# Kernel optimization log

Measured on AMD Instinct MI355X. Metric: run time of the kernel, lower is better.

Reference implementation:

```python
import jax, jax.numpy as jnp
import numpy as np

B, N, F_IN, H, C = 32768, 12, 128, 4, 64  # batch, nodes/graph, input_dim, heads, hidden_dim
NEG_SLOPE = 0.2  # PyG GATConv default leaky_relu slope


def setup_inputs() -> dict:
    key = jax.random.key(0)
    ks = jax.random.split(key, 16)
    def xavier(k, shape):
        fan_in, fan_out = shape[0], int(np.prod(shape[1:]))
        lim = float(np.sqrt(6.0 / (fan_in + fan_out)))
        return jax.random.uniform(k, shape, jnp.float32, -lim, lim)
    return {
        "node_features": jax.random.normal(ks[0], (B, N, F_IN), jnp.float32),
        "W1": xavier(ks[1], (F_IN, H, C)),
        "a_src1": xavier(ks[2], (H, C)),
        "a_dst1": xavier(ks[3], (H, C)),
        "b1": jnp.zeros((H * C,), jnp.float32),
        "W2": xavier(ks[4], (H * C, 1, C)),
        "a_src2": xavier(ks[5], (1, C)),
        "a_dst2": xavier(ks[6], (1, C)),
        "b2": jnp.zeros((C,), jnp.float32),
        # classifier head: 64 -> 32 -> 1
        "Wc1": xavier(ks[7], (C, C // 2)),
        "bc1": jnp.zeros((C // 2,), jnp.float32),
        "Wc2": xavier(ks[8], (C // 2, 1)),
        "bc2": jnp.zeros((1,), jnp.float32),
    }


def gat_dense(x, W, a_src, a_dst, bias, concat):
    # x: [B, N, F].  Fully-connected graph + self-loops (PyG GATConv default)
    # == dense attention over all N nodes of each graph.
    h = jnp.einsum("bnf,fhc->bnhc", x, W)               # [B,N,H,C]
    e_src = jnp.einsum("bnhc,hc->bnh", h, a_src)         # alpha contrib of source j
    e_dst = jnp.einsum("bnhc,hc->bnh", h, a_dst)         # alpha contrib of target i
    # edge (j -> i): logit = leaky_relu(e_dst[i] + e_src[j])
    logits = jax.nn.leaky_relu(e_dst[:, :, None, :] + e_src[:, None, :, :], NEG_SLOPE)  # [B,i,j,H]
    alpha = jax.nn.softmax(logits, axis=2)               # softmax over neighbors j
    out = jnp.einsum("bijh,bjhc->bihc", alpha, h)        # aggregate
    if concat:
        out = out.reshape(out.shape[0], out.shape[1], -1)
    else:
        out = out.mean(axis=2)
    return out + bias


def reference(node_features, W1, a_src1, a_dst1, b1, W2, a_src2, a_dst2, b2,
              Wc1, bc1, Wc2, bc2):
    # eval mode: dropouts are identity; is_finetune=False so finetune_block skipped
    x = jax.nn.elu(gat_dense(node_features, W1, a_src1, a_dst1, b1, concat=True))   # [B,N,256]
    x = jax.nn.elu(gat_dense(x, W2, a_src2, a_dst2, b2, concat=False))              # [B,N,64]
    g = x.mean(axis=1)                                                              # global_mean_pool -> [B,64]
    hdn = jax.nn.relu(g @ Wc1 + bc1)
    logits = hdn @ Wc2 + bc2                                                        # [B,1]
    return logits
```

## Files before the change

### kernel.cpp

```cpp
#include <hip/hip_runtime.h>
#include <math.h>

typedef __attribute__((ext_vector_type(8))) short bf16x8;
typedef __attribute__((ext_vector_type(4))) float f32x4;

namespace {
constexpr int NN  = 12;
constexpr int FIN = 128;
constexpr int D1  = 256;
constexpr int C2  = 64;
constexpr float SLOPE = 0.2f;

__device__ __forceinline__ unsigned short f2bf(float f) {
    unsigned u = __builtin_bit_cast(unsigned, f);
    u += 0x7FFFu + ((u >> 16) & 1u);
    return (unsigned short)(u >> 16);
}
__device__ __forceinline__ float elu1(float x) { return x > 0.f ? x : __expf(x) - 1.f; }
__device__ __forceinline__ float lrelu(float x) { return x > 0.f ? x : SLOPE * x; }
}

__global__ void prep_weights(const float* __restrict__ W1, const float* __restrict__ as1,
                             const float* __restrict__ ad1,
                             const float* __restrict__ W2, const float* __restrict__ as2,
                             const float* __restrict__ ad2,
                             unsigned short* __restrict__ wsB1, unsigned short* __restrict__ wsB2) {
    int t = blockIdx.x * 256 + threadIdx.x;
    if (t < 34816) {
        int i = t & 7, l = (t >> 3) & 63, kn = t >> 9;
        int kt = kn / 17, nt = kn % 17;
        int k = kt * 32 + (l >> 4) * 8 + i;
        float v = 0.f;
        if (nt < 16) {
            v = W1[k * 256 + nt * 16 + (l & 15)];
        } else {
            int cc = l & 15;
            if (cc < 4)      for (int c = 0; c < 64; ++c) v += W1[k * 256 + cc * 64 + c] * as1[cc * 64 + c];
            else if (cc < 8) for (int c = 0; c < 64; ++c) v += W1[k * 256 + (cc - 4) * 64 + c] * ad1[(cc - 4) * 64 + c];
        }
        wsB1[t] = f2bf(v);
    } else if (t < 55296) {
        int t2 = t - 34816;
        int i = t2 & 7, l = (t2 >> 3) & 63, kn = t2 >> 9;
        int kt = kn / 5, nt = kn % 5;
        int k = kt * 32 + (l >> 4) * 8 + i;
        float v = 0.f;
        if (nt < 4) {
            v = W2[k * 64 + nt * 16 + (l & 15)];
        } else {
            int cc = l & 15;
            if (cc == 0)      for (int c = 0; c < 64; ++c) v += W2[k * 64 + c] * as2[c];
            else if (cc == 1) for (int c = 0; c < 64; ++c) v += W2[k * 64 + c] * ad2[c];
        }
        wsB2[t2] = f2bf(v);
    }
}

__global__ __launch_bounds__(256, 2) void gat_mfma5(
    const float* __restrict__ x_in,
    const unsigned short* __restrict__ wsB1,
    const unsigned short* __restrict__ wsB2,
    const float* __restrict__ b1, const float* __restrict__ b2,
    const float* __restrict__ Wc1, const float* __restrict__ bc1,
    const float* __restrict__ Wc2, const float* __restrict__ bc2,
    float* __restrict__ out)
{
    __shared__ __align__(16) unsigned char R0[13056];
    __shared__ __align__(16) unsigned char R1[32768];
    __shared__ __align__(16) unsigned char R2[24576];
    __shared__ float eS1[48][4], eD1[48][4];
    __shared__ float eS2[48], eD2[48];
    __shared__ float gpool[4][64];

    const int b = blockIdx.x, t = threadIdx.x;
    const int w = t >> 6, l = t & 63, l15 = l & 15, lq = l >> 4;

    {
        const float4* xs = (const float4*)(x_in + (size_t)b * (4 * NN * FIN));
        #pragma unroll
        for (int it = 0; it < 6; ++it) {
            int q = t + 256 * it;
            float4 v = xs[q];
            int e0 = q << 2, r = e0 >> 7, k = e0 & 127;
            int addr = ((r << 8) + (k << 1)) ^ ((r & 7) << 4);
            unsigned p0 = (unsigned)f2bf(v.x) | ((unsigned)f2bf(v.y) << 16);
            unsigned p1 = (unsigned)f2bf(v.z) | ((unsigned)f2bf(v.w) << 16);
            *(uint2*)(R0 + addr) = make_uint2(p0, p1);
        }
        #pragma unroll
        for (int it = 0; it < 6; ++it)
            *(uint4*)(R2 + ((it * 256 + t) << 4)) = make_uint4(0, 0, 0, 0);
        #pragma unroll
        for (int z = 0; z < 2; ++z) {
            int id = t + 256 * z;
            int col = id >> 1, bs = 6 + (id & 1);
            int addr = ((col << 7) + (bs << 4)) ^ ((col & 7) << 4);
            *(uint4*)(R1 + addr) = make_uint4(0, 0, 0, 0);
        }
    }
    __syncthreads();

    {
        const uint4* pb = (const uint4*)wsB1;
        bf16x8 Bf[4][4];
        #pragma unroll
        for (int ng = 0; ng < 4; ++ng)
            #pragma unroll
            for (int kt = 0; kt < 4; ++kt)
                Bf[ng][kt] = __builtin_bit_cast(bf16x8, pb[(kt * 17 + (w * 4 + ng)) * 64 + l]);
        bf16x8 Bfe[4];
        if (w == 0) {
            #pragma unroll
            for (int kt = 0; kt < 4; ++kt)
                Bfe[kt] = __builtin_bit_cast(bf16x8, pb[(kt * 17 + 16) * 64 + l]);
        }
        #pragma unroll
        for (int m = 0; m < 3; ++m) {
            int r = m * 16 + l15, abase = (r << 8) + (lq << 4), swz = (r & 7) << 4;
            bf16x8 Af[4];
            #pragma unroll
            for (int kt = 0; kt < 4; ++kt)
                Af[kt] = *(const bf16x8*)(R0 + ((abase + (kt << 6)) ^ swz));
            f32x4 acc[4];
            #pragma unroll
            for (int ng = 0; ng < 4; ++ng) acc[ng] = (f32x4){0.f, 0.f, 0.f, 0.f};
            #pragma unroll
            for (int ng = 0; ng < 4; ++ng)
                #pragma unroll
                for (int kt = 0; kt < 4; ++kt)
                    acc[ng] = __builtin_amdgcn_mfma_f32_16x16x32_bf16(Af[kt], Bf[ng][kt], acc[ng], 0, 0, 0);
            int row0 = m * 16 + lq * 4;
            #pragma unroll
            for (int ng = 0; ng < 4; ++ng) {
                int col = w * 64 + ng * 16 + l15;
                unsigned q0 = (unsigned)f2bf(acc[ng][0]) | ((unsigned)f2bf(acc[ng][1]) << 16);
                unsigned q1 = (unsigned)f2bf(acc[ng][2]) | ((unsigned)f2bf(acc[ng][3]) << 16);
                int addr = ((col << 7) + (row0 << 1)) ^ ((col & 7) << 4);
                *(uint2*)(R1 + addr) = make_uint2(q0, q1);
            }
            if (w == 0) {
                f32x4 acce = (f32x4){0.f, 0.f, 0.f, 0.f};
                #pragma unroll
                for (int kt = 0; kt < 4; ++kt)
                    acce = __builtin_amdgcn_mfma_f32_16x16x32_bf16(Af[kt], Bfe[kt], acce, 0, 0, 0);
                if (l15 < 8) {
                    #pragma unroll
                    for (int reg = 0; reg < 4; ++reg) {
                        int row = row0 + reg;
                        if (l15 < 4) eS1[row][l15] = acce[reg];
                        else         eD1[row][l15 - 4] = acce[reg];
                    }
                }
            }
        }
    }
    __syncthreads();

    if (t < 192) {
        int g = t / 48, rem = t % 48, i = rem >> 2, h = rem & 3;
        int rowi = g * 12 + i;
        float edi = eD1[rowi][h];
        float lv[12]; float mx = -1e30f;
        #pragma unroll
        for (int j = 0; j < 12; ++j) {
            float v = lrelu(edi + eS1[g * 12 + j][h]);
            lv[j] = v; mx = fmaxf(mx, v);
        }
        float s = 0.f;
        #pragma unroll
        for (int j = 0; j < 12; ++j) { lv[j] = __expf(lv[j] - mx); s += lv[j]; }
        float inv = 1.f / s;
        unsigned char* base = R2 + h * 6144;
        int rb = rowi << 7, swz = (rowi & 7) << 4, ob = g * 24;
        #pragma unroll
        for (int p = 0; p < 3; ++p) {
            unsigned q0 = (unsigned)f2bf(lv[4*p]   * inv) | ((unsigned)f2bf(lv[4*p+1] * inv) << 16);
            unsigned q1 = (unsigned)f2bf(lv[4*p+2] * inv) | ((unsigned)f2bf(lv[4*p+3] * inv) << 16);
            int addr = (rb + ob + p * 8) ^ swz;
            *(uint2*)(base + addr) = make_uint2(q0, q1);
        }
    }
    __syncthreads();

    {
        bf16x8 Bh[2][4];
        #pragma unroll
        for (int kt = 0; kt < 2; ++kt)
            #pragma unroll
            for (int nt = 0; nt < 4; ++nt) {
                int col = w * 64 + nt * 16 + l15;
                int addr = ((col << 7) + (kt << 6) + (lq << 4)) ^ ((col & 7) << 4);
                Bh[kt][nt] = *(const bf16x8*)(R1 + addr);
            }
        float b1v[4];
        #pragma unroll
        for (int nt = 0; nt < 4; ++nt) b1v[nt] = b1[w * 64 + nt * 16 + l15];
        unsigned char* aab = R2 + w * 6144;
        #pragma unroll
        for (int m = 0; m < 3; ++m) {
            int r = m * 16 + l15, swz = (r & 7) << 4;
            bf16x8 Aa[2];
            #pragma unroll
            for (int kt = 0; kt < 2; ++kt)
                Aa[kt] = *(const bf16x8*)(aab + (((r << 7) + (kt << 6) + (lq << 4)) ^ swz));
            #pragma unroll
            for (int nt = 0; nt < 4; ++nt) {
                f32x4 acc = (f32x4){0.f, 0.f, 0.f, 0.f};
                #pragma unroll
                for (int kt = 0; kt < 2; ++kt)
                    acc = __builtin_amdgcn_mfma_f32_16x16x32_bf16(Aa[kt], Bh[kt][nt], acc, 0, 0, 0);
                #pragma unroll
                for (int reg = 0; reg < 4; ++reg) {
                    int row = m * 16 + lq * 4 + reg;
                    float val = elu1(acc[reg] + b1v[nt]);
                    int addr = ((row << 7) + ((nt * 16 + l15) << 1)) ^ ((row & 7) << 4);
                    *(unsigned short*)(aab + addr) = f2bf(val);
                }
            }
        }
    }
    __syncthreads();

    {
        if (t < 128) {
            int col = t >> 1, bs = 6 + (t & 1);
            int addr = ((col << 7) + (bs << 4)) ^ ((col & 7) << 4);
            *(uint4*)(R1 + addr) = make_uint4(0, 0, 0, 0);
        }
        if (t < 192) {
            *(uint4*)(R1 + 8192 + (t << 4)) = make_uint4(0, 0, 0, 0);
            *(uint4*)(R1 + 8192 + ((t + 192) << 4)) = make_uint4(0, 0, 0, 0);
        }
        const uint4* pb2 = (const uint4*)wsB2;
        bf16x8 Bg[8], Be2[8];
        #pragma unroll
        for (int kt = 0; kt < 8; ++kt)
            Bg[kt] = __builtin_bit_cast(bf16x8, pb2[(kt * 5 + w) * 64 + l]);
        if (w == 0) {
            #pragma unroll
            for (int kt = 0; kt < 8; ++kt)
                Be2[kt] = __builtin_bit_cast(bf16x8, pb2[(kt * 5 + 4) * 64 + l]);
        }
        #pragma unroll
        for (int m = 0; m < 3; ++m) {
            int r = m * 16 + l15, swz = (r & 7) << 4;
            f32x4 acc = (f32x4){0.f, 0.f, 0.f, 0.f}, acce = (f32x4){0.f, 0.f, 0.f, 0.f};
            #pragma unroll
            for (int kt = 0; kt < 8; ++kt) {
                int addr = (kt >> 1) * 6144 + (((r << 7) + ((kt & 1) << 6) + (lq << 4)) ^ swz);
                bf16x8 Ax = *(const bf16x8*)(R2 + addr);
                acc = __builtin_amdgcn_mfma_f32_16x16x32_bf16(Ax, Bg[kt], acc, 0, 0, 0);
                if (w == 0) acce = __builtin_amdgcn_mfma_f32_16x16x32_bf16(Ax, Be2[kt], acce, 0, 0, 0);
            }
            int col = w * 16 + l15, row0 = m * 16 + lq * 4;
            unsigned q0 = (unsigned)f2bf(acc[0]) | ((unsigned)f2bf(acc[1]) << 16);
            unsigned q1 = (unsigned)f2bf(acc[2]) | ((unsigned)f2bf(acc[3]) << 16);
            int addr = ((col << 7) + (row0 << 1)) ^ ((col & 7) << 4);
            *(uint2*)(R1 + addr) = make_uint2(q0, q1);
            if (w == 0 && l15 < 2) {
                #pragma unroll
                for (int reg = 0; reg < 4; ++reg) {
                    int row = row0 + reg;
                    if (l15 == 0) eS2[row] = acce[reg];
                    else          eD2[row] = acce[reg];
                }
            }
        }
    }
    __syncthreads();

    if (t < 48) {
        int g = t / 12;
        float edi = eD2[t];
        float lv[12]; float mx = -1e30f;
        #pragma unroll
        for (int j = 0; j < 12; ++j) {
            float v = lrelu(edi + eS2[g * 12 + j]);
            lv[j] = v; mx = fmaxf(mx, v);
        }
        float s = 0.f;
        #pragma unroll
        for (int j = 0; j < 12; ++j) { lv[j] = __expf(lv[j] - mx); s += lv[j]; }
        float inv = 1.f / s;
        int rb = t << 7, swz = (t & 7) << 4, ob = g * 24;
        #pragma unroll
        for (int p = 0; p < 3; ++p) {
            unsigned q0 = (unsigned)f2bf(lv[4*p]   * inv) | ((unsigned)f2bf(lv[4*p+1] * inv) << 16);
            unsigned q1 = (unsigned)f2bf(lv[4*p+2] * inv) | ((unsigned)f2bf(lv[4*p+3] * inv) << 16);
            int addr = 8192 + ((rb + ob + p * 8) ^ swz);
            *(uint2*)(R1 + addr) = make_uint2(q0, q1);
        }
    }
    __syncthreads();

    {
        bf16x8 Bh2[2];
        int col = w * 16 + l15;
        #pragma unroll
        for (int kt = 0; kt < 2; ++kt) {
            int addr = ((col << 7) + (kt << 6) + (lq << 4)) ^ ((col & 7) << 4);
            Bh2[kt] = *(const bf16x8*)(R1 + addr);
        }
        float b2v = b2[col];
        #pragma unroll
        for (int m = 0; m < 3; ++m) {
            int r = m * 16 + l15, swz = (r & 7) << 4;
            f32x4 acc = (f32x4){0.f, 0.f, 0.f, 0.f};
            #pragma unroll
            for (int kt = 0; kt < 2; ++kt) {
                bf16x8 Aa = *(const bf16x8*)(R1 + 8192 + (((r << 7) + (kt << 6) + (lq << 4)) ^ swz));
                acc = __builtin_amdgcn_mfma_f32_16x16x32_bf16(Aa, Bh2[kt], acc, 0, 0, 0);
            }
            #pragma unroll
            for (int reg = 0; reg < 4; ++reg) {
                int row = m * 16 + lq * 4 + reg;
                *(float*)(R0 + row * 272 + (col << 2)) = elu1(acc[reg] + b2v);
            }
        }
    }
    __syncthreads();

    {
        int o = t & 63, g = t >> 6;
        float s = 0.f;
        #pragma unroll
        for (int j = 0; j < 12; ++j)
            s += *(const float*)(R0 + (g * 12 + j) * 272 + (o << 2));
        gpool[g][o] = s * (1.0f / 12.0f);
    }
    __syncthreads();

    if (t < 128) {
        int g = t >> 5, nr = t & 31;
        float acc = bc1[nr];
        #pragma unroll
        for (int cc = 0; cc < 64; ++cc)
            acc = fmaf(gpool[g][cc], Wc1[cc * 32 + nr], acc);
        float val = fmaxf(acc, 0.f) * Wc2[nr];
        #pragma unroll
        for (int msk = 1; msk < 32; msk <<= 1) val += __shfl_xor(val, msk);
        if (nr == 0) out[b * 4 + g] = val + bc2[0];
    }
}

__global__ __launch_bounds__(256, 4) void gat_fused_f32(
    const float* __restrict__ x_in, const float* __restrict__ W1,
    const float* __restrict__ a_src1, const float* __restrict__ a_dst1,
    const float* __restrict__ b1, const float* __restrict__ W2,
    const float* __restrict__ a_src2, const float* __restrict__ a_dst2,
    const float* __restrict__ b2, const float* __restrict__ Wc1,
    const float* __restrict__ bc1, const float* __restrict__ Wc2,
    const float* __restrict__ bc2, float* __restrict__ out)
{
    __shared__ union {
        float x_l[NN][FIN];
        struct { float h2[NN][C2]; float x3[NN][C2]; } s2;
    } u;
    __shared__ float h1s[NN][D1];
    __shared__ float x2s[NN][D1];
    __shared__ float alpha1[NN][NN][4];
    __shared__ float e_s1[NN][4], e_d1[NN][4];
    __shared__ float e_s2[NN], e_d2[NN];
    __shared__ float alpha2[NN][NN];
    __shared__ float gph[C2];
    __shared__ float hdn[32];

    const int b = blockIdx.x, t = threadIdx.x;
    const float* xb = x_in + (size_t)b * (NN * FIN);
    for (int i = t; i < NN * FIN; i += 256) (&u.x_l[0][0])[i] = xb[i];
    __syncthreads();
    {
        const int o0 = (t & 127) * 2, n0 = (t >> 7) * 6;
        float acc[6][2];
        #pragma unroll
        for (int i = 0; i < 6; ++i) { acc[i][0] = 0.f; acc[i][1] = 0.f; }
        for (int f = 0; f < FIN; f += 4) {
            float4 xv[6];
            #pragma unroll
            for (int i = 0; i < 6; ++i) xv[i] = *(const float4*)&u.x_l[n0 + i][f];
            #pragma unroll
            for (int k = 0; k < 4; ++k) {
                const float2 wv = *(const float2*)&W1[(f + k) * D1 + o0];
                #pragma unroll
                for (int i = 0; i < 6; ++i) {
                    const float xs = ((const float*)&xv[i])[k];
                    acc[i][0] = fmaf(xs, wv.x, acc[i][0]);
                    acc[i][1] = fmaf(xs, wv.y, acc[i][1]);
                }
            }
        }
        #pragma unroll
        for (int i = 0; i < 6; ++i) { h1s[n0+i][o0] = acc[i][0]; h1s[n0+i][o0+1] = acc[i][1]; }
    }
    __syncthreads();
    if (t < NN * 4) {
        const int n = t >> 2, h = t & 3;
        float es = 0.f, ed = 0.f;
        for (int c = 0; c < 64; ++c) {
            const float v = h1s[n][h * 64 + c];
            es = fmaf(v, a_src1[h * 64 + c], es);
            ed = fmaf(v, a_dst1[h * 64 + c], ed);
        }
        e_s1[n][h] = es; e_d1[n][h] = ed;
    }
    __syncthreads();
    if (t < NN * 4) {
        const int i = t >> 2, h = t & 3;
        const float edi = e_d1[i][h];
        float lv[NN]; float m = -1e30f;
        #pragma unroll
        for (int j = 0; j < NN; ++j) {
            float v = edi + e_s1[j][h]; v = v > 0.f ? v : SLOPE * v;
            lv[j] = v; m = fmaxf(m, v);
        }
        float s = 0.f;
        #pragma unroll
        for (int j = 0; j < NN; ++j) { lv[j] = __expf(lv[j] - m); s += lv[j]; }
        const float inv = 1.f / s;
        #pragma unroll
        for (int j = 0; j < NN; ++j) alpha1[i][j][h] = lv[j] * inv;
    }
    __syncthreads();
    {
        const int o = t, h = o >> 6;
        const float bo = b1[o];
        float v[NN];
        #pragma unroll
        for (int j = 0; j < NN; ++j) v[j] = h1s[j][o];
        #pragma unroll
        for (int i = 0; i < NN; ++i) {
            float acc = 0.f;
            #pragma unroll
            for (int j = 0; j < NN; ++j) acc = fmaf(alpha1[i][j][h], v[j], acc);
            x2s[i][o] = acc + bo > 0.f ? acc + bo : expm1f(acc + bo);
        }
    }
    __syncthreads();
    {
        const int c = t & 63, n0 = (t >> 6) * 3;
        float acc[3] = {0.f, 0.f, 0.f};
        for (int f = 0; f < D1; f += 4) {
            float4 xv[3];
            #pragma unroll
            for (int i = 0; i < 3; ++i) xv[i] = *(const float4*)&x2s[n0 + i][f];
            #pragma unroll
            for (int k = 0; k < 4; ++k) {
                const float wv = W2[(f + k) * C2 + c];
                #pragma unroll
                for (int i = 0; i < 3; ++i) acc[i] = fmaf(((const float*)&xv[i])[k], wv, acc[i]);
            }
        }
        #pragma unroll
        for (int i = 0; i < 3; ++i) u.s2.h2[n0 + i][c] = acc[i];
    }
    __syncthreads();
    if (t < NN) {
        float es = 0.f, ed = 0.f;
        for (int c = 0; c < 64; c += 4) {
            const float4 v  = *(const float4*)&u.s2.h2[t][c];
            const float4 as = *(const float4*)&a_src2[c];
            const float4 ad = *(const float4*)&a_dst2[c];
            es += v.x*as.x + v.y*as.y + v.z*as.z + v.w*as.w;
            ed += v.x*ad.x + v.y*ad.y + v.z*ad.z + v.w*ad.w;
        }
        e_s2[t] = es; e_d2[t] = ed;
    }
    __syncthreads();
    if (t < NN) {
        const float edi = e_d2[t];
        float lv[NN]; float m = -1e30f;
        #pragma unroll
        for (int j = 0; j < NN; ++j) {
            float v = edi + e_s2[j]; v = v > 0.f ? v : SLOPE * v;
            lv[j] = v; m = fmaxf(m, v);
        }
        float s = 0.f;
        #pragma unroll
        for (int j = 0; j < NN; ++j) { lv[j] = __expf(lv[j] - m); s += lv[j]; }
        const float inv = 1.f / s;
        #pragma unroll
        for (int j = 0; j < NN; ++j) alpha2[t][j] = lv[j] * inv;
    }
    __syncthreads();
    {
        const int c = t & 63, i0 = (t >> 6) * 3;
        float v[NN];
        #pragma unroll
        for (int j = 0; j < NN; ++j) v[j] = u.s2.h2[j][c];
        const float bc = b2[c];
        #pragma unroll
        for (int ii = 0; ii < 3; ++ii) {
            const int i = i0 + ii;
            float acc = 0.f;
            #pragma unroll
            for (int j = 0; j < NN; ++j) acc = fmaf(alpha2[i][j], v[j], acc);
            u.s2.x3[i][c] = acc + bc > 0.f ? acc + bc : expm1f(acc + bc);
        }
    }
    __syncthreads();
    if (t < C2) {
        float s = 0.f;
        #pragma unroll
        for (int i = 0; i < NN; ++i) s += u.s2.x3[i][t];
        gph[t] = s * (1.0f / NN);
    }
    __syncthreads();
    if (t < 32) {
        float acc = bc1[t];
        for (int c = 0; c < C2; ++c) acc = fmaf(gph[c], Wc1[c * 32 + t], acc);
        hdn[t] = fmaxf(acc, 0.f);
    }
    __syncthreads();
    if (t == 0) {
        float acc = bc2[0];
        #pragma unroll
        for (int k = 0; k < 32; ++k) acc = fmaf(hdn[k], Wc2[k], acc);
        out[b] = acc;
    }
}

extern "C" void kernel_launch(void* const* d_in, const int* in_sizes, int n_in,
                              void* d_out, int out_size, void* d_ws, size_t ws_size,
                              hipStream_t stream) {
    const float* x   = (const float*)d_in[0];
    const float* W1  = (const float*)d_in[1];
    const float* as1 = (const float*)d_in[2];
    const float* ad1 = (const float*)d_in[3];
    const float* b1  = (const float*)d_in[4];
    const float* W2  = (const float*)d_in[5];
    const float* as2 = (const float*)d_in[6];
    const float* ad2 = (const float*)d_in[7];
    const float* b2  = (const float*)d_in[8];
    const float* Wc1 = (const float*)d_in[9];
    const float* bc1 = (const float*)d_in[10];
    const float* Wc2 = (const float*)d_in[11];
    const float* bc2 = (const float*)d_in[12];
    float* out = (float*)d_out;

    const int B = in_sizes[0] / (NN * FIN);

    if (ws_size >= 110592 && (B % 4) == 0) {
        unsigned short* wsB1 = (unsigned short*)d_ws;
        unsigned short* wsB2 = wsB1 + 34816;
        prep_weights<<<216, 256, 0, stream>>>(W1, as1, ad1, W2, as2, ad2, wsB1, wsB2);
        gat_mfma5<<<B / 4, 256, 0, stream>>>(x, wsB1, wsB2, b1, b2, Wc1, bc1, Wc2, bc2, out);
    } else {
        gat_fused_f32<<<B, 256, 0, stream>>>(x, W1, as1, ad1, b1, W2, as2, ad2, b2,
                                             Wc1, bc1, Wc2, bc2, out);
    }
}
```

Before: 169.2 us.

## Split per-block GAT work across eight waves instead of four

Moves the fused GAT kernel from 256 to 512 threads per block and redistributes every MFMA stage across the eight waves. Layer-1 column groups are split in half per wave, the aggregation step buffers A fragments and adds a barrier before writing back in place, and layer-2's fifteen (tile,row) units are spread two per wave. The goal is more waves per block for better latency hiding and shorter per-wave serial MFMA chains. In exchange it adds a barrier, leaves some waves idle in later stages, and may hurt occupancy through register and LDS limits under the new launch bounds.

```diff
diff --git a/kernel.cpp b/kernel.cpp
--- a/kernel.cpp
+++ b/kernel.cpp
@@ -56,7 +56,7 @@
     }
 }
 
-__global__ __launch_bounds__(256, 2) void gat_mfma5(
+__global__ __launch_bounds__(512, 4) void gat_mfma6(
     const float* __restrict__ x_in,
     const unsigned short* __restrict__ wsB1,
     const unsigned short* __restrict__ wsB2,
@@ -78,8 +78,8 @@
     {
         const float4* xs = (const float4*)(x_in + (size_t)b * (4 * NN * FIN));
         #pragma unroll
-        for (int it = 0; it < 6; ++it) {
-            int q = t + 256 * it;
+        for (int it = 0; it < 3; ++it) {
+            int q = t + 512 * it;
             float4 v = xs[q];
             int e0 = q << 2, r = e0 >> 7, k = e0 & 127;
             int addr = ((r << 8) + (k << 1)) ^ ((r & 7) << 4);
@@ -88,12 +88,10 @@
             *(uint2*)(R0 + addr) = make_uint2(p0, p1);
         }
         #pragma unroll
-        for (int it = 0; it < 6; ++it)
-            *(uint4*)(R2 + ((it * 256 + t) << 4)) = make_uint4(0, 0, 0, 0);
-        #pragma unroll
-        for (int z = 0; z < 2; ++z) {
-            int id = t + 256 * z;
-            int col = id >> 1, bs = 6 + (id & 1);
+        for (int it = 0; it < 3; ++it)
+            *(uint4*)(R2 + ((it * 512 + t) << 4)) = make_uint4(0, 0, 0, 0);
+        {
+            int col = t >> 1, bs = 6 + (t & 1);
             int addr = ((col << 7) + (bs << 4)) ^ ((col & 7) << 4);
             *(uint4*)(R1 + addr) = make_uint4(0, 0, 0, 0);
         }
@@ -102,12 +100,13 @@
 
     {
         const uint4* pb = (const uint4*)wsB1;
-        bf16x8 Bf[4][4];
-        #pragma unroll
-        for (int ng = 0; ng < 4; ++ng)
+        const int h = w >> 1, half = w & 1;
+        bf16x8 Bf[2][4];
+        #pragma unroll
+        for (int ngl = 0; ngl < 2; ++ngl)
             #pragma unroll
             for (int kt = 0; kt < 4; ++kt)
-                Bf[ng][kt] = __builtin_bit_cast(bf16x8, pb[(kt * 17 + (w * 4 + ng)) * 64 + l]);
+                Bf[ngl][kt] = __builtin_bit_cast(bf16x8, pb[(kt * 17 + (h * 4 + half * 2 + ngl)) * 64 + l]);
         bf16x8 Bfe[4];
         if (w == 0) {
             #pragma unroll
@@ -121,20 +120,20 @@
             #pragma unroll
             for (int kt = 0; kt < 4; ++kt)
                 Af[kt] = *(const bf16x8*)(R0 + ((abase + (kt << 6)) ^ swz));
-            f32x4 acc[4];
-            #pragma unroll
-            for (int ng = 0; ng < 4; ++ng) acc[ng] = (f32x4){0.f, 0.f, 0.f, 0.f};
-            #pragma unroll
-            for (int ng = 0; ng < 4; ++ng)
+            f32x4 acc[2];
+            #pragma unroll
+            for (int ngl = 0; ngl < 2; ++ngl) acc[ngl] = (f32x4){0.f, 0.f, 0.f, 0.f};
+            #pragma unroll
+            for (int ngl = 0; ngl < 2; ++ngl)
                 #pragma unroll
                 for (int kt = 0; kt < 4; ++kt)
-                    acc[ng] = __builtin_amdgcn_mfma_f32_16x16x32_bf16(Af[kt], Bf[ng][kt], acc[ng], 0, 0, 0);
+                    acc[ngl] = __builtin_amdgcn_mfma_f32_16x16x32_bf16(Af[kt], Bf[ngl][kt], acc[ngl], 0, 0, 0);
             int row0 = m * 16 + lq * 4;
             #pragma unroll
-            for (int ng = 0; ng < 4; ++ng) {
-                int col = w * 64 + ng * 16 + l15;
-                unsigned q0 = (unsigned)f2bf(acc[ng][0]) | ((unsigned)f2bf(acc[ng][1]) << 16);
-                unsigned q1 = (unsigned)f2bf(acc[ng][2]) | ((unsigned)f2bf(acc[ng][3]) << 16);
+            for (int ngl = 0; ngl < 2; ++ngl) {
+                int col = h * 64 + (half * 2 + ngl) * 16 + l15;
+                unsigned q0 = (unsigned)f2bf(acc[ngl][0]) | ((unsigned)f2bf(acc[ngl][1]) << 16);
+                unsigned q1 = (unsigned)f2bf(acc[ngl][2]) | ((unsigned)f2bf(acc[ngl][3]) << 16);
                 int addr = ((col << 7) + (row0 << 1)) ^ ((col & 7) << 4);
                 *(uint2*)(R1 + addr) = make_uint2(q0, q1);
             }
@@ -183,37 +182,42 @@
     __syncthreads();
 
     {
-        bf16x8 Bh[2][4];
+        const int h = w >> 1, half = w & 1;
+        bf16x8 Bh[2][2];
         #pragma unroll
         for (int kt = 0; kt < 2; ++kt)
             #pragma unroll
-            for (int nt = 0; nt < 4; ++nt) {
-                int col = w * 64 + nt * 16 + l15;
+            for (int ntl = 0; ntl < 2; ++ntl) {
+                int col = h * 64 + (half * 2 + ntl) * 16 + l15;
                 int addr = ((col << 7) + (kt << 6) + (lq << 4)) ^ ((col & 7) << 4);
-                Bh[kt][nt] = *(const bf16x8*)(R1 + addr);
-            }
-        float b1v[4];
-        #pragma unroll
-        for (int nt = 0; nt < 4; ++nt) b1v[nt] = b1[w * 64 + nt * 16 + l15];
-        unsigned char* aab = R2 + w * 6144;
+                Bh[kt][ntl] = *(const bf16x8*)(R1 + addr);
+            }
+        float b1v[2];
+        #pragma unroll
+        for (int ntl = 0; ntl < 2; ++ntl) b1v[ntl] = b1[h * 64 + (half * 2 + ntl) * 16 + l15];
+        unsigned char* aab = R2 + h * 6144;
+        bf16x8 Aa[3][2];
         #pragma unroll
         for (int m = 0; m < 3; ++m) {
             int r = m * 16 + l15, swz = (r & 7) << 4;
-            bf16x8 Aa[2];
             #pragma unroll
             for (int kt = 0; kt < 2; ++kt)
-                Aa[kt] = *(const bf16x8*)(aab + (((r << 7) + (kt << 6) + (lq << 4)) ^ swz));
-            #pragma unroll
-            for (int nt = 0; nt < 4; ++nt) {
+                Aa[m][kt] = *(const bf16x8*)(aab + (((r << 7) + (kt << 6) + (lq << 4)) ^ swz));
+        }
+        __syncthreads();
+        #pragma unroll
+        for (int m = 0; m < 3; ++m) {
+            #pragma unroll
+            for (int ntl = 0; ntl < 2; ++ntl) {
                 f32x4 acc = (f32x4){0.f, 0.f, 0.f, 0.f};
                 #pragma unroll
                 for (int kt = 0; kt < 2; ++kt)
-                    acc = __builtin_amdgcn_mfma_f32_16x16x32_bf16(Aa[kt], Bh[kt][nt], acc, 0, 0, 0);
+                    acc = __builtin_amdgcn_mfma_f32_16x16x32_bf16(Aa[m][kt], Bh[kt][ntl], acc, 0, 0, 0);
                 #pragma unroll
                 for (int reg = 0; reg < 4; ++reg) {
                     int row = m * 16 + lq * 4 + reg;
-                    float val = elu1(acc[reg] + b1v[nt]);
-                    int addr = ((row << 7) + ((nt * 16 + l15) << 1)) ^ ((row & 7) << 4);
+                    float val = elu1(acc[reg] + b1v[ntl]);
+                    int addr = ((row << 7) + (((half * 2 + ntl) * 16 + l15) << 1)) ^ ((row & 7) << 4);
                     *(unsigned short*)(aab + addr) = f2bf(val);
                 }
             }
@@ -232,37 +236,37 @@
             *(uint4*)(R1 + 8192 + ((t + 192) << 4)) = make_uint4(0, 0, 0, 0);
         }
         const uint4* pb2 = (const uint4*)wsB2;
-        bf16x8 Bg[8], Be2[8];
-        #pragma unroll
-        for (int kt = 0; kt < 8; ++kt)
-            Bg[kt] = __builtin_bit_cast(bf16x8, pb2[(kt * 5 + w) * 64 + l]);
-        if (w == 0) {
-            #pragma unroll
-            for (int kt = 0; kt < 8; ++kt)
-                Be2[kt] = __builtin_bit_cast(bf16x8, pb2[(kt * 5 + 4) * 64 + l]);
-        }
-        #pragma unroll
-        for (int m = 0; m < 3; ++m) {
-            int r = m * 16 + l15, swz = (r & 7) << 4;
-            f32x4 acc = (f32x4){0.f, 0.f, 0.f, 0.f}, acce = (f32x4){0.f, 0.f, 0.f, 0.f};
-            #pragma unroll
-            for (int kt = 0; kt < 8; ++kt) {
-                int addr = (kt >> 1) * 6144 + (((r << 7) + ((kt & 1) << 6) + (lq << 4)) ^ swz);
-                bf16x8 Ax = *(const bf16x8*)(R2 + addr);
-                acc = __builtin_amdgcn_mfma_f32_16x16x32_bf16(Ax, Bg[kt], acc, 0, 0, 0);
-                if (w == 0) acce = __builtin_amdgcn_mfma_f32_16x16x32_bf16(Ax, Be2[kt], acce, 0, 0, 0);
-            }
-            int col = w * 16 + l15, row0 = m * 16 + lq * 4;
-            unsigned q0 = (unsigned)f2bf(acc[0]) | ((unsigned)f2bf(acc[1]) << 16);
-            unsigned q1 = (unsigned)f2bf(acc[2]) | ((unsigned)f2bf(acc[3]) << 16);
-            int addr = ((col << 7) + (row0 << 1)) ^ ((col & 7) << 4);
-            *(uint2*)(R1 + addr) = make_uint2(q0, q1);
-            if (w == 0 && l15 < 2) {
-                #pragma unroll
-                for (int reg = 0; reg < 4; ++reg) {
-                    int row = row0 + reg;
-                    if (l15 == 0) eS2[row] = acce[reg];
-                    else          eD2[row] = acce[reg];
+        #pragma unroll
+        for (int ui = 0; ui < 2; ++ui) {
+            int u = w * 2 + ui;
+            if (u < 15) {
+                int tile = u / 3, m = u % 3;
+                bf16x8 Bg[8];
+                #pragma unroll
+                for (int kt = 0; kt < 8; ++kt)
+                    Bg[kt] = __builtin_bit_cast(bf16x8, pb2[(kt * 5 + tile) * 64 + l]);
+                int r = m * 16 + l15, swz = (r & 7) << 4;
+                f32x4 acc = (f32x4){0.f, 0.f, 0.f, 0.f};
+                #pragma unroll
+                for (int kt = 0; kt < 8; ++kt) {
+                    int addr = (kt >> 1) * 6144 + (((r << 7) + ((kt & 1) << 6) + (lq << 4)) ^ swz);
+                    bf16x8 Ax = *(const bf16x8*)(R2 + addr);
+                    acc = __builtin_amdgcn_mfma_f32_16x16x32_bf16(Ax, Bg[kt], acc, 0, 0, 0);
+                }
+                int row0 = m * 16 + lq * 4;
+                if (tile < 4) {
+                    int col = tile * 16 + l15;
+                    unsigned q0 = (unsigned)f2bf(acc[0]) | ((unsigned)f2bf(acc[1]) << 16);
+                    unsigned q1 = (unsigned)f2bf(acc[2]) | ((unsigned)f2bf(acc[3]) << 16);
+                    int addr = ((col << 7) + (row0 << 1)) ^ ((col & 7) << 4);
+                    *(uint2*)(R1 + addr) = make_uint2(q0, q1);
+                } else if (l15 < 2) {
+                    #pragma unroll
+                    for (int reg = 0; reg < 4; ++reg) {
+                        int row = row0 + reg;
+                        if (l15 == 0) eS2[row] = acc[reg];
+                        else          eD2[row] = acc[reg];
+                    }
                 }
             }
         }
@@ -294,16 +298,18 @@
     __syncthreads();
 
     {
+        const int otile = w & 3;
         bf16x8 Bh2[2];
-        int col = w * 16 + l15;
+        int col = otile * 16 + l15;
         #pragma unroll
         for (int kt = 0; kt < 2; ++kt) {
             int addr = ((col << 7) + (kt << 6) + (lq << 4)) ^ ((col & 7) << 4);
             Bh2[kt] = *(const bf16x8*)(R1 + addr);
         }
         float b2v = b2[col];
-        #pragma unroll
-        for (int m = 0; m < 3; ++m) {
+        const int m0 = (w < 4) ? 0 : 2, mcount = (w < 4) ? 2 : 1;
+        for (int mi = 0; mi < mcount; ++mi) {
+            int m = m0 + mi;
             int r = m * 16 + l15, swz = (r & 7) << 4;
             f32x4 acc = (f32x4){0.f, 0.f, 0.f, 0.f};
             #pragma unroll
@@ -320,7 +326,7 @@
     }
     __syncthreads();
 
-    {
+    if (t < 256) {
         int o = t & 63, g = t >> 6;
         float s = 0.f;
         #pragma unroll
@@ -543,7 +549,7 @@
         unsigned short* wsB1 = (unsigned short*)d_ws;
         unsigned short* wsB2 = wsB1 + 34816;
         prep_weights<<<216, 256, 0, stream>>>(W1, as1, ad1, W2, as2, ad2, wsB1, wsB2);
-        gat_mfma5<<<B / 4, 256, 0, stream>>>(x, wsB1, wsB2, b1, b2, Wc1, bc1, Wc2, bc2, out);
+        gat_mfma6<<<B / 4, 512, 0, stream>>>(x, wsB1, wsB2, b1, b2, Wc1, bc1, Wc2, bc2, out);
     } else {
         gat_fused_f32<<<B, 256, 0, stream>>>(x, W1, as1, ad1, b1, W2, as2, ad2, b2,
                                              Wc1, bc1, Wc2, bc2, out);
```

Result: faster. 155.8 us (-7.9%).
